# Performance work log

Measured on AMD Instinct MI355X. Metric: run time of the kernel, lower is better.

## Reference

```python
import jax, jax.numpy as jnp
import numpy as np

WINDOW = 1024  # sliding-window mask_mod: attend to keys within WINDOW behind the query


def setup_inputs() -> dict:
    key = jax.random.key(0)
    B, L, H, E = 2, 2048, 16, 64
    qkv = jax.random.normal(key, (B, L, 3, H, E), dtype=jnp.float32)
    return {"qkv": qkv}


def reference(qkv) -> jnp.ndarray:
    # Training path of FlexAttention.forward (key_cache/val_cache/cache_seqlens = None).
    B, L, _, H, E = qkv.shape
    q = qkv[:, :, 0]  # [b, l, h, e]
    k = qkv[:, :, 1]
    v = qkv[:, :, 2]

    scale = 1.0 / (E ** 0.5)  # flex_attention default softmax scaling
    scores = jnp.einsum("bqhe,bkhe->bhqk", q, k) * scale  # [b, h, q, kv]

    q_idx = jnp.arange(L)[:, None]
    kv_idx = jnp.arange(L)[None, :]
    dist = q_idx - kv_idx  # [q, kv]

    # score_mod: ALiBi bias, slope_h = 2^(-8*(h+1)/H)
    slopes = jnp.exp2(-8.0 * (jnp.arange(H, dtype=jnp.float32) + 1.0) / H)
    scores = scores - slopes[None, :, None, None] * dist.astype(jnp.float32)

    # and_masks(mask_mod, causal_mask): sliding window AND causal
    mask = (dist >= 0) & (dist < WINDOW)  # causal guarantees >=1 valid key per row
    scores = jnp.where(mask[None, None], scores, -jnp.inf)

    attn = jax.nn.softmax(scores, axis=-1)
    out = jnp.einsum("bhqk,bkhe->bqhe", attn, v)  # [b, l, h, e]
    return out
```

## Files before the change

kernel.cpp:

```cpp
#include <hip/hip_runtime.h>
#include <cstdint>

#define L_SEQ 2048
#define NH 16
#define EDIM 64
#define WINDOW 1024
#define QT 64
#define KT 64
#define LOG2E 1.4426950408889634f
#define M_FIX 16.0f

typedef short bf16x8 __attribute__((ext_vector_type(8)));
typedef short bf16x4 __attribute__((ext_vector_type(4)));
typedef float f32x4 __attribute__((ext_vector_type(4)));

__device__ __forceinline__ short f2bf(float x) {
    uint32_t u = __builtin_bit_cast(uint32_t, x);
    uint32_t r = (u + 0x7fffu + ((u >> 16) & 1u)) >> 16;
    return (short)(r & 0xffffu);
}
__device__ __forceinline__ short f2bf_trunc(float x) {
    return (short)(__builtin_bit_cast(uint32_t, x) >> 16);
}

__device__ __forceinline__ f32x4 mfma16(bf16x4 a, bf16x4 b, f32x4 c) {
#if __has_builtin(__builtin_amdgcn_mfma_f32_16x16x16bf16_1k)
    return __builtin_amdgcn_mfma_f32_16x16x16bf16_1k(a, b, c, 0, 0, 0);
#else
    asm("s_nop 1\n\tv_mfma_f32_16x16x16_bf16 %0, %1, %2, %0"
        : "+v"(c) : "v"(a), "v"(b));
    return c;
#endif
}

__device__ __forceinline__ void async16(const short* g, const short* l) {
    __builtin_amdgcn_global_load_lds(
        (const __attribute__((address_space(1))) void*)(uintptr_t)(g),
        (__attribute__((address_space(3))) void*)(uintptr_t)(l),
        16, 0, 0);
}

#define SYNC_VMCNT4()                                           \
    do {                                                        \
        asm volatile("s_waitcnt vmcnt(4)" ::: "memory");        \
        __builtin_amdgcn_s_barrier();                           \
        __builtin_amdgcn_sched_barrier(0);                      \
    } while (0)

__global__ __launch_bounds__(256) void prepass4(const float* __restrict__ qkv,
        short* __restrict__ kw, short* __restrict__ vw) {
    __shared__ float vt[64][68];
    const int x = blockIdx.x;
    const int xcd = x & 7, y = x >> 3;
    const int pairid = xcd * 4 + (y >> 5);
    const int tile = y & 31;
    const int b = pairid >> 4, h = pairid & 15;
    const int tid = threadIdx.x;
    const int tg = pairid * 32 + tile;
    const float* base = qkv + (size_t)b * (L_SEQ * 3072) + (size_t)tile * 64 * 3072 + h * 64;
    short* ko = kw + (size_t)tg * 4096;
    short* vo = vw + (size_t)tg * 4096;

    #pragma unroll
    for (int it = 0; it < 2; ++it) {
        const int c = tid + it * 256;
        const int row = c >> 3, cc = (c & 7) ^ (row & 7);
        const float* src = base + (size_t)row * 3072 + 1024 + cc * 8;
        float4 a = *(const float4*)src, d = *(const float4*)(src + 4);
        short* o = ko + (size_t)c * 8;
        o[0] = f2bf(a.x); o[1] = f2bf(a.y); o[2] = f2bf(a.z); o[3] = f2bf(a.w);
        o[4] = f2bf(d.x); o[5] = f2bf(d.y); o[6] = f2bf(d.z); o[7] = f2bf(d.w);
    }
    {
        const int row = tid >> 2, e0 = (tid & 3) << 4;
        const float* src = base + (size_t)row * 3072 + 2048 + e0;
        #pragma unroll
        for (int q4 = 0; q4 < 4; ++q4) {
            float4 a = *(const float4*)(src + q4 * 4);
            vt[e0 + q4 * 4 + 0][row] = a.x;
            vt[e0 + q4 * 4 + 1][row] = a.y;
            vt[e0 + q4 * 4 + 2][row] = a.z;
            vt[e0 + q4 * 4 + 3][row] = a.w;
        }
    }
    __syncthreads();
    #pragma unroll
    for (int it = 0; it < 2; ++it) {
        const int c = tid + it * 256;
        const int et = c >> 7, a = (c >> 6) & 1, l6 = c & 63;
        const int quad = l6 >> 4, r16 = l6 & 15;
        const int e = et * 16 + r16;
        float4 x0 = *(const float4*)&vt[e][a * 32 + quad * 4];
        float4 x1 = *(const float4*)&vt[e][a * 32 + 16 + quad * 4];
        bf16x8 o8;
        o8[0] = f2bf(x0.x); o8[1] = f2bf(x0.y); o8[2] = f2bf(x0.z); o8[3] = f2bf(x0.w);
        o8[4] = f2bf(x1.x); o8[5] = f2bf(x1.y); o8[6] = f2bf(x1.z); o8[7] = f2bf(x1.w);
        *(bf16x8*)(vo + (size_t)c * 8) = o8;
    }
}

__global__ __launch_bounds__(256, 4) void flexattn_fwd8(
        const float* __restrict__ qkv, const short* __restrict__ kw,
        const short* __restrict__ vw, float* __restrict__ out) {
    __shared__ __align__(16) short kB[3][4096];
    __shared__ __align__(16) short vB2[2][4096];

    const int s = blockIdx.y & 31;
    const int k = blockIdx.y >> 5;
    const int t16 = (s + ((k >> 1) << 4)) & 31;
    const int qtile = (k & 1) ? (31 - t16) : t16;
    const int pairid = blockIdx.x * 4 + k;
    const int h = pairid & 15;
    const int b = pairid >> 4;

    const int tid   = threadIdx.x;
    const int w     = tid >> 6;
    const int lane  = tid & 63;
    const int quad  = lane >> 4;
    const int r16   = lane & 15;
    const int qhalf = w & 1;
    const int khalf = w >> 1;
    const int qb    = qtile * QT;
    const int bh32  = (b * NH + h) * 32;
    const int q0    = qb + qhalf * 32 + r16;

    const int t0q = (qb >= WINDOW - 1) ? ((qb - (WINDOW - 1)) >> 6) : 0;
    const int t1  = qtile;
    const int swz = quad ^ (r16 & 7);
    const int cb0 = w * 128;

    float4 qraw[2][2][2];
    #pragma unroll
    for (int g = 0; g < 2; ++g) {
        const float* qrow = qkv + (size_t)b * (L_SEQ * 3072)
                                + (size_t)(q0 + g * 16) * 3072 + h * 64;
        #pragma unroll
        for (int es = 0; es < 2; ++es) {
            const float* p = qrow + es * 32 + quad * 8;
            qraw[g][es][0] = *(const float4*)p;
            qraw[g][es][1] = *(const float4*)(p + 4);
        }
    }

    {
        const int t0c1 = (t0q + 1 <= t1) ? t0q + 1 : t1;
        const short* k0t = kw + (size_t)(bh32 + t0q) * 4096;
        const short* k1t = kw + (size_t)(bh32 + t0c1) * 4096;
        const short* v0t = vw + (size_t)(bh32 + t0q) * 4096;
        short* kd0 = &kB[t0q % 3][0];
        short* kd1 = &kB[(t0q + 1) % 3][0];
        short* vd0 = &vB2[t0q & 1][0];
        async16(k0t + (size_t)(cb0 + lane) * 8,      kd0 + (size_t)cb0 * 8);
        async16(k0t + (size_t)(cb0 + 64 + lane) * 8, kd0 + (size_t)(cb0 + 64) * 8);
        async16(k1t + (size_t)(cb0 + lane) * 8,      kd1 + (size_t)cb0 * 8);
        async16(k1t + (size_t)(cb0 + 64 + lane) * 8, kd1 + (size_t)(cb0 + 64) * 8);
        async16(v0t + (size_t)(cb0 + lane) * 8,      vd0 + (size_t)cb0 * 8);
        async16(v0t + (size_t)(cb0 + 64 + lane) * 8, vd0 + (size_t)(cb0 + 64) * 8);
    }

    const float qscale = 0.125f * LOG2E;
    bf16x8 qfrag[2][2];
    #pragma unroll
    for (int g = 0; g < 2; ++g) {
        #pragma unroll
        for (int es = 0; es < 2; ++es) {
            float4 a = qraw[g][es][0];
            float4 c = qraw[g][es][1];
            bf16x8 f;
            f[0] = f2bf(a.x * qscale); f[1] = f2bf(a.y * qscale);
            f[2] = f2bf(a.z * qscale); f[3] = f2bf(a.w * qscale);
            f[4] = f2bf(c.x * qscale); f[5] = f2bf(c.y * qscale);
            f[6] = f2bf(c.z * qscale); f[7] = f2bf(c.w * qscale);
            qfrag[g][es] = f;
        }
    }

    const float slope2 = __builtin_amdgcn_exp2f(-8.0f * (float)(h + 1) / (float)NH) * LOG2E;
    const float c64 = slope2 * 64.0f;
    f32x4 EA[2][2];
    #pragma unroll
    for (int g = 0; g < 2; ++g)
        #pragma unroll
        for (int ctl = 0; ctl < 2; ++ctl)
            #pragma unroll
            for (int r = 0; r < 4; ++r)
                EA[g][ctl][r] = slope2 * (float)(t0q * 64 + (khalf * 2 + ctl) * 16
                                                 + quad * 4 + r - (q0 + g * 16)) - M_FIX;

    f32x4 O[2][4] = {};
    float rs[2] = {0.f, 0.f};

    for (int kt = t0q; kt <= t1; ++kt) {
        const int kc = kt % 3;
        const int vc = kt & 1;

        SYNC_VMCNT4();

        {
            const int kpre = (kt + 2 <= t1) ? kt + 2 : t1;
            const int vpre = (kt + 1 <= t1) ? kt + 1 : t1;
            short* kd = &kB[(kt + 2) % 3][0];
            short* vd = &vB2[(kt + 1) & 1][0];
            const short* ktile = kw + (size_t)(bh32 + kpre) * 4096;
            const short* vtile = vw + (size_t)(bh32 + vpre) * 4096;
            async16(ktile + (size_t)(cb0 + lane) * 8,      kd + (size_t)cb0 * 8);
            async16(ktile + (size_t)(cb0 + 64 + lane) * 8, kd + (size_t)(cb0 + 64) * 8);
            async16(vtile + (size_t)(cb0 + lane) * 8,      vd + (size_t)cb0 * 8);
            async16(vtile + (size_t)(cb0 + 64 + lane) * 8, vd + (size_t)(cb0 + 64) * 8);
        }

        f32x4 S[2][2];
        __builtin_amdgcn_s_setprio(1);
        #pragma unroll
        for (int ctl = 0; ctl < 2; ++ctl) {
            const int ct = khalf * 2 + ctl;
            const int c0 = ((ct * 16 + r16) << 3) + swz;
            bf16x8 k0 = *(const bf16x8*)&kB[kc][c0 * 8];
            bf16x8 k1 = *(const bf16x8*)&kB[kc][(c0 ^ 4) * 8];
            #pragma unroll
            for (int g = 0; g < 2; ++g) {
                f32x4 acc = __builtin_amdgcn_mfma_f32_16x16x32_bf16(k0, qfrag[g][0], EA[g][ctl], 0, 0, 0);
                S[g][ctl] = __builtin_amdgcn_mfma_f32_16x16x32_bf16(k1, qfrag[g][1], acc, 0, 0, 0);
            }
        }
        __builtin_amdgcn_s_setprio(0);

        bf16x4 pb[2][2];
        if (kt != t0q && kt != t1) {
            #pragma unroll
            for (int g = 0; g < 2; ++g)
                #pragma unroll
                for (int ctl = 0; ctl < 2; ++ctl)
                    #pragma unroll
                    for (int r = 0; r < 4; ++r) {
                        const float pe = __builtin_amdgcn_exp2f(S[g][ctl][r]);
                        rs[g] += pe;
                        pb[g][ctl][r] = f2bf_trunc(pe);
                    }
        } else {
            const int key0 = kt * 64 + khalf * 32 + quad * 4;
            #pragma unroll
            for (int g = 0; g < 2; ++g) {
                const int qg = q0 + g * 16;
                #pragma unroll
                for (int ctl = 0; ctl < 2; ++ctl)
                    #pragma unroll
                    for (int r = 0; r < 4; ++r) {
                        const int dist = qg - (key0 + ctl * 16 + r);
                        float pe = __builtin_amdgcn_exp2f(S[g][ctl][r]);
                        pe = (dist < 0 || dist >= WINDOW) ? 0.0f : pe;
                        rs[g] += pe;
                        pb[g][ctl][r] = f2bf_trunc(pe);
                    }
            }
        }

        SYNC_VMCNT4();

        __builtin_amdgcn_s_setprio(1);
        #pragma unroll
        for (int et = 0; et < 4; ++et) {
            bf16x8 v8 = *(const bf16x8*)&vB2[vc][(size_t)((et * 2 + khalf) * 64 + lane) * 8];
            bf16x4 vlo = {v8[0], v8[1], v8[2], v8[3]};
            bf16x4 vhi = {v8[4], v8[5], v8[6], v8[7]};
            #pragma unroll
            for (int g = 0; g < 2; ++g) {
                O[g][et] = mfma16(vlo, pb[g][0], O[g][et]);
                O[g][et] = mfma16(vhi, pb[g][1], O[g][et]);
            }
        }
        __builtin_amdgcn_s_setprio(0);

        #pragma unroll
        for (int ctl = 0; ctl < 2; ++ctl) {
            EA[0][ctl] += c64;
            EA[1][ctl] += c64;
        }
    }

    __syncthreads();
    float* oS = (float*)&kB[0][0];
    float* rS = (float*)&vB2[0][0];
    if (khalf) {
        float* dst = oS + qhalf * 2048;
        #pragma unroll
        for (int g = 0; g < 2; ++g)
            #pragma unroll
            for (int et = 0; et < 4; ++et)
                #pragma unroll
                for (int j = 0; j < 4; ++j)
                    dst[((g * 4 + et) * 4 + j) * 64 + lane] = O[g][et][j];
        rS[qhalf * 128 + lane]      = rs[0];
        rS[qhalf * 128 + 64 + lane] = rs[1];
    }
    __syncthreads();
    if (!khalf) {
        const float* src = oS + qhalf * 2048;
        #pragma unroll
        for (int g = 0; g < 2; ++g)
            #pragma unroll
            for (int et = 0; et < 4; ++et)
                #pragma unroll
                for (int j = 0; j < 4; ++j)
                    O[g][et][j] += src[((g * 4 + et) * 4 + j) * 64 + lane];
        rs[0] += rS[qhalf * 128 + lane];
        rs[1] += rS[qhalf * 128 + 64 + lane];

        #pragma unroll
        for (int g = 0; g < 2; ++g) {
            float r = rs[g];
            r += __shfl_xor(r, 16, 64);
            r += __shfl_xor(r, 32, 64);
            const float rl = 1.0f / r;
            float* op = out + ((size_t)b * L_SEQ + (q0 + g * 16)) * (NH * EDIM) + h * EDIM;
            #pragma unroll
            for (int et = 0; et < 4; ++et) {
                float4 o4 = {O[g][et][0] * rl, O[g][et][1] * rl,
                             O[g][et][2] * rl, O[g][et][3] * rl};
                *(float4*)(op + et * 16 + quad * 4) = o4;
            }
        }
    }
}

__global__ __launch_bounds__(256, 2) void flexattn_fwd_fb(
        const float* __restrict__ qkv, float* __restrict__ out) {
    __shared__ __align__(16) short kT[KT * 72];
    __shared__ __align__(16) short vB[8 * 64 * 8];
    __shared__ __align__(16) short pT[4][16 * 72];

    const int qtile = blockIdx.x;
    const int h     = blockIdx.y;
    const int b     = blockIdx.z;
    const int tid   = threadIdx.x;
    const int w     = tid >> 6;
    const int lane  = tid & 63;
    const int quad  = lane >> 4;
    const int r16   = lane & 15;
    const int qb = qtile * QT;
    const int rowstride = 3 * NH * EDIM;

    const float* qbase = qkv + ((size_t)b * L_SEQ * 3 + 0) * (NH * EDIM) + h * EDIM;
    const float* kbase = qkv + ((size_t)b * L_SEQ * 3 + 1) * (NH * EDIM) + h * EDIM;
    const float* vbase = qkv + ((size_t)b * L_SEQ * 3 + 2) * (NH * EDIM) + h * EDIM;

    const float qscale = 0.125f * LOG2E;
    bf16x8 qfrag[2];
    {
        const int qg = qb + w * 16 + r16;
        const float* qrow = qbase + (size_t)qg * rowstride;
        #pragma unroll
        for (int es = 0; es < 2; ++es) {
            const float* p = qrow + es * 32 + quad * 8;
            float4 a = *(const float4*)p;
            float4 c = *(const float4*)(p + 4);
            bf16x8 f;
            f[0] = f2bf(a.x * qscale); f[1] = f2bf(a.y * qscale);
            f[2] = f2bf(a.z * qscale); f[3] = f2bf(a.w * qscale);
            f[4] = f2bf(c.x * qscale); f[5] = f2bf(c.y * qscale);
            f[6] = f2bf(c.z * qscale); f[7] = f2bf(c.w * qscale);
            qfrag[es] = f;
        }
    }

    const float slope2 = __builtin_amdgcn_exp2f(-8.0f * (float)(h + 1) / (float)NH) * LOG2E;
    f32x4 O[4] = {{0,0,0,0},{0,0,0,0},{0,0,0,0},{0,0,0,0}};
    float m_run[4] = {-1e30f, -1e30f, -1e30f, -1e30f};
    float l_run[4] = {0.f, 0.f, 0.f, 0.f};

    const int kmin = (qb >= WINDOW - 1) ? (qb - (WINDOW - 1)) : 0;
    const int t0 = kmin >> 6;
    const int t1 = qtile;

    for (int kt = t0; kt <= t1; ++kt) {
        __syncthreads();
        {
            const int j = tid >> 2;
            const int ebase = (tid & 3) * 16;
            const float* krow = kbase + (size_t)(kt * KT + j) * rowstride + ebase;
            const float* vrow = vbase + (size_t)(kt * KT + j) * rowstride + ebase;
            const int js = j >> 5, qd = (j >> 3) & 3, ii = j & 7;
            #pragma unroll
            for (int ee = 0; ee < 4; ++ee) {
                const int e = ebase + ee * 4;
                float4 k4 = *(const float4*)(krow + ee * 4);
                short* kd = &kT[j * 72 + e];
                kd[0] = f2bf(k4.x); kd[1] = f2bf(k4.y);
                kd[2] = f2bf(k4.z); kd[3] = f2bf(k4.w);
                float4 v4 = *(const float4*)(vrow + ee * 4);
                const int et = e >> 4;
                const int ln = qd * 16 + (e & 15);
                short* vd = &vB[(((js * 4 + et) * 64) + ln) * 8 + ii];
                vd[0]  = f2bf(v4.x);
                vd[8]  = f2bf(v4.y);
                vd[16] = f2bf(v4.z);
                vd[24] = f2bf(v4.w);
            }
        }
        __syncthreads();

        f32x4 S[4];
        #pragma unroll
        for (int ct = 0; ct < 4; ++ct) {
            const short* kr = &kT[(ct * 16 + r16) * 72 + quad * 8];
            bf16x8 b0 = *(const bf16x8*)kr;
            bf16x8 b1 = *(const bf16x8*)(kr + 32);
            f32x4 acc = {0.f, 0.f, 0.f, 0.f};
            acc = __builtin_amdgcn_mfma_f32_16x16x32_bf16(qfrag[0], b0, acc, 0, 0, 0);
            acc = __builtin_amdgcn_mfma_f32_16x16x32_bf16(qfrag[1], b1, acc, 0, 0, 0);
            S[ct] = acc;
        }

        const int q0 = qb + w * 16 + quad * 4;
        float p[4][4];
        float mt[4] = {-1e30f, -1e30f, -1e30f, -1e30f};
        #pragma unroll
        for (int ct = 0; ct < 4; ++ct) {
            const int kg = kt * KT + ct * 16 + r16;
            #pragma unroll
            for (int r = 0; r < 4; ++r) {
                const int dist = q0 + r - kg;
                float s2 = S[ct][r] - slope2 * (float)dist;
                if (dist < 0 || dist >= WINDOW) s2 = -1e30f;
                p[ct][r] = s2;
                mt[r] = fmaxf(mt[r], s2);
            }
        }
        #pragma unroll
        for (int d = 1; d < 16; d <<= 1) {
            #pragma unroll
            for (int r = 0; r < 4; ++r)
                mt[r] = fmaxf(mt[r], __shfl_xor(mt[r], d, 64));
        }

        float alpha[4], rsum[4];
        #pragma unroll
        for (int r = 0; r < 4; ++r) {
            const float mn = fmaxf(m_run[r], mt[r]);
            alpha[r] = __builtin_amdgcn_exp2f(m_run[r] - mn);
            m_run[r] = mn;
            float sacc = 0.f;
            #pragma unroll
            for (int ct = 0; ct < 4; ++ct) {
                const float pe = __builtin_amdgcn_exp2f(p[ct][r] - mn);
                p[ct][r] = pe;
                sacc += pe;
            }
            rsum[r] = sacc;
        }
        #pragma unroll
        for (int d = 1; d < 16; d <<= 1) {
            #pragma unroll
            for (int r = 0; r < 4; ++r)
                rsum[r] += __shfl_xor(rsum[r], d, 64);
        }
        #pragma unroll
        for (int r = 0; r < 4; ++r)
            l_run[r] = l_run[r] * alpha[r] + rsum[r];
        #pragma unroll
        for (int et = 0; et < 4; ++et) {
            #pragma unroll
            for (int r = 0; r < 4; ++r)
                O[et][r] *= alpha[r];
        }

        short* pw = &pT[w][0];
        #pragma unroll
        for (int ct = 0; ct < 4; ++ct) {
            #pragma unroll
            for (int r = 0; r < 4; ++r)
                pw[(quad * 4 + r) * 72 + ct * 16 + r16] = f2bf(p[ct][r]);
        }
        bf16x8 aP0 = *(const bf16x8*)(pw + r16 * 72 + quad * 8);
        bf16x8 aP1 = *(const bf16x8*)(pw + r16 * 72 + 32 + quad * 8);

        #pragma unroll
        for (int et = 0; et < 4; ++et) {
            bf16x8 v0 = *(const bf16x8*)(&vB[((0 * 4 + et) * 64 + lane) * 8]);
            O[et] = __builtin_amdgcn_mfma_f32_16x16x32_bf16(aP0, v0, O[et], 0, 0, 0);
            bf16x8 v1 = *(const bf16x8*)(&vB[((1 * 4 + et) * 64 + lane) * 8]);
            O[et] = __builtin_amdgcn_mfma_f32_16x16x32_bf16(aP1, v1, O[et], 0, 0, 0);
        }
    }

    float* obase = out + (((size_t)b * L_SEQ) * NH + (size_t)h) * EDIM;
    #pragma unroll
    for (int r = 0; r < 4; ++r) {
        const int qg = qb + w * 16 + quad * 4 + r;
        const float rl = 1.0f / l_run[r];
        float* orow = obase + (size_t)qg * (NH * EDIM);
        #pragma unroll
        for (int et = 0; et < 4; ++et)
            orow[et * 16 + r16] = O[et][r] * rl;
    }
}

extern "C" void kernel_launch(void* const* d_in, const int* in_sizes, int n_in,
                              void* d_out, int out_size, void* d_ws, size_t ws_size,
                              hipStream_t stream) {
    const float* qkv = (const float*)d_in[0];
    float* out = (float*)d_out;
    const size_t need = (size_t)2 * 1024 * 4096 * sizeof(short);
    if (ws_size >= need) {
        short* kw = (short*)d_ws;
        short* vw = kw + (size_t)1024 * 4096;
        prepass4<<<1024, 256, 0, stream>>>(qkv, kw, vw);
        dim3 grid(8, 128);
        flexattn_fwd8<<<grid, 256, 0, stream>>>(qkv, kw, vw, out);
    } else {
        dim3 gridfb(L_SEQ / QT, NH, 2);
        flexattn_fwd_fb<<<gridfb, 256, 0, stream>>>(qkv, out);
    }
}
```

Baseline: 113.4 us.

## Use persistent 512-thread blocks with atomic work queue and 4-way key split

The attention kernel becomes persistent. Each 512-thread block pulls (head-pair, query-tile) work items from a per-XCD atomic counter, longest tiles first, and the prepass resets the counters. Within a block, eight waves split each 64-key tile four ways instead of two, so each wave does half as many MFMAs per tile, and partial outputs are combined through a two-stage LDS reduction. The aim is better load balance across the triangular sliding-window workload and more latency hiding per CU, at the cost of extra reduction passes, barriers and atomic traffic.

```diff
diff --git a/kernel.cpp b/kernel.cpp
--- a/kernel.cpp
+++ b/kernel.cpp
@@ -40,17 +40,18 @@
         16, 0, 0);
 }
 
-#define SYNC_VMCNT4()                                           \
+#define SYNC_VMCNT2()                                           \
     do {                                                        \
-        asm volatile("s_waitcnt vmcnt(4)" ::: "memory");        \
+        asm volatile("s_waitcnt vmcnt(2)" ::: "memory");        \
         __builtin_amdgcn_s_barrier();                           \
         __builtin_amdgcn_sched_barrier(0);                      \
     } while (0)
 
-__global__ __launch_bounds__(256) void prepass4(const float* __restrict__ qkv,
-        short* __restrict__ kw, short* __restrict__ vw) {
+__global__ __launch_bounds__(256) void prepass5(const float* __restrict__ qkv,
+        short* __restrict__ kw, short* __restrict__ vw, int* __restrict__ cnt) {
     __shared__ float vt[64][68];
     const int x = blockIdx.x;
+    if (x < 8 && threadIdx.x == 0) cnt[x] = 0;
     const int xcd = x & 7, y = x >> 3;
     const int pairid = xcd * 4 + (y >> 5);
     const int tile = y & 31;
@@ -99,225 +100,233 @@
     }
 }
 
-__global__ __launch_bounds__(256, 4) void flexattn_fwd8(
+__global__ __launch_bounds__(512, 4) void flexattn_fwd10(
         const float* __restrict__ qkv, const short* __restrict__ kw,
-        const short* __restrict__ vw, float* __restrict__ out) {
-    __shared__ __align__(16) short kB[3][4096];
-    __shared__ __align__(16) short vB2[2][4096];
-
-    const int s = blockIdx.y & 31;
-    const int k = blockIdx.y >> 5;
-    const int t16 = (s + ((k >> 1) << 4)) & 31;
-    const int qtile = (k & 1) ? (31 - t16) : t16;
-    const int pairid = blockIdx.x * 4 + k;
-    const int h = pairid & 15;
-    const int b = pairid >> 4;
-
-    const int tid   = threadIdx.x;
-    const int w     = tid >> 6;
-    const int lane  = tid & 63;
-    const int quad  = lane >> 4;
-    const int r16   = lane & 15;
+        const short* __restrict__ vw, int* __restrict__ cnt,
+        float* __restrict__ out) {
+    __shared__ __align__(16) short smem[5 * 4096];
+    __shared__ int itemS;
+    short (*kB)[4096]  = (short (*)[4096])&smem[0];
+    short (*vB2)[4096] = (short (*)[4096])&smem[3 * 4096];
+
+    const int xq   = blockIdx.x;
+    const int tid  = threadIdx.x;
+    const int w    = tid >> 6;
+    const int lane = tid & 63;
+    const int quad = lane >> 4;
+    const int r16  = lane & 15;
     const int qhalf = w & 1;
-    const int khalf = w >> 1;
-    const int qb    = qtile * QT;
-    const int bh32  = (b * NH + h) * 32;
-    const int q0    = qb + qhalf * 32 + r16;
-
-    const int t0q = (qb >= WINDOW - 1) ? ((qb - (WINDOW - 1)) >> 6) : 0;
-    const int t1  = qtile;
-    const int swz = quad ^ (r16 & 7);
-    const int cb0 = w * 128;
-
-    float4 qraw[2][2][2];
-    #pragma unroll
-    for (int g = 0; g < 2; ++g) {
-        const float* qrow = qkv + (size_t)b * (L_SEQ * 3072)
-                                + (size_t)(q0 + g * 16) * 3072 + h * 64;
-        #pragma unroll
-        for (int es = 0; es < 2; ++es) {
-            const float* p = qrow + es * 32 + quad * 8;
-            qraw[g][es][0] = *(const float4*)p;
-            qraw[g][es][1] = *(const float4*)(p + 4);
-        }
-    }
-
-    {
-        const int t0c1 = (t0q + 1 <= t1) ? t0q + 1 : t1;
-        const short* k0t = kw + (size_t)(bh32 + t0q) * 4096;
-        const short* k1t = kw + (size_t)(bh32 + t0c1) * 4096;
-        const short* v0t = vw + (size_t)(bh32 + t0q) * 4096;
-        short* kd0 = &kB[t0q % 3][0];
-        short* kd1 = &kB[(t0q + 1) % 3][0];
-        short* vd0 = &vB2[t0q & 1][0];
-        async16(k0t + (size_t)(cb0 + lane) * 8,      kd0 + (size_t)cb0 * 8);
-        async16(k0t + (size_t)(cb0 + 64 + lane) * 8, kd0 + (size_t)(cb0 + 64) * 8);
-        async16(k1t + (size_t)(cb0 + lane) * 8,      kd1 + (size_t)cb0 * 8);
-        async16(k1t + (size_t)(cb0 + 64 + lane) * 8, kd1 + (size_t)(cb0 + 64) * 8);
-        async16(v0t + (size_t)(cb0 + lane) * 8,      vd0 + (size_t)cb0 * 8);
-        async16(v0t + (size_t)(cb0 + 64 + lane) * 8, vd0 + (size_t)(cb0 + 64) * 8);
-    }
-
-    const float qscale = 0.125f * LOG2E;
-    bf16x8 qfrag[2][2];
-    #pragma unroll
-    for (int g = 0; g < 2; ++g) {
-        #pragma unroll
-        for (int es = 0; es < 2; ++es) {
-            float4 a = qraw[g][es][0];
-            float4 c = qraw[g][es][1];
-            bf16x8 f;
-            f[0] = f2bf(a.x * qscale); f[1] = f2bf(a.y * qscale);
-            f[2] = f2bf(a.z * qscale); f[3] = f2bf(a.w * qscale);
-            f[4] = f2bf(c.x * qscale); f[5] = f2bf(c.y * qscale);
-            f[6] = f2bf(c.z * qscale); f[7] = f2bf(c.w * qscale);
-            qfrag[g][es] = f;
-        }
-    }
-
-    const float slope2 = __builtin_amdgcn_exp2f(-8.0f * (float)(h + 1) / (float)NH) * LOG2E;
-    const float c64 = slope2 * 64.0f;
-    f32x4 EA[2][2];
-    #pragma unroll
-    for (int g = 0; g < 2; ++g)
-        #pragma unroll
-        for (int ctl = 0; ctl < 2; ++ctl)
+    const int kq    = w >> 1;
+    const int swz  = quad ^ (r16 & 7);
+    const int cb0  = w * 64;
+
+    for (;;) {
+        if (tid == 0) itemS = atomicAdd(&cnt[xq], 1);
+        __syncthreads();
+        const int item = itemS;
+        if (item >= 128) return;
+
+        const int pairid = xq * 4 + (item & 3);
+        const int qtile  = 31 - (item >> 2);
+        const int h  = pairid & 15;
+        const int b  = pairid >> 4;
+        const int qb = qtile * QT;
+        const int bh32 = pairid * 32;
+        const int q0 = qb + qhalf * 32 + r16;
+        const int t0q = (qb >= WINDOW - 1) ? ((qb - (WINDOW - 1)) >> 6) : 0;
+        const int t1  = qtile;
+
+        float4 qraw[2][2][2];
+        #pragma unroll
+        for (int g = 0; g < 2; ++g) {
+            const float* qrow = qkv + (size_t)b * (L_SEQ * 3072)
+                                    + (size_t)(q0 + g * 16) * 3072 + h * 64;
+            #pragma unroll
+            for (int es = 0; es < 2; ++es) {
+                const float* p = qrow + es * 32 + quad * 8;
+                qraw[g][es][0] = *(const float4*)p;
+                qraw[g][es][1] = *(const float4*)(p + 4);
+            }
+        }
+
+        {
+            const int t0c1 = (t0q + 1 <= t1) ? t0q + 1 : t1;
+            const short* k0t = kw + (size_t)(bh32 + t0q) * 4096;
+            const short* k1t = kw + (size_t)(bh32 + t0c1) * 4096;
+            const short* v0t = vw + (size_t)(bh32 + t0q) * 4096;
+            async16(k0t + (size_t)(cb0 + lane) * 8, &kB[t0q % 3][cb0 * 8]);
+            async16(k1t + (size_t)(cb0 + lane) * 8, &kB[(t0q + 1) % 3][cb0 * 8]);
+            async16(v0t + (size_t)(cb0 + lane) * 8, &vB2[t0q & 1][cb0 * 8]);
+        }
+
+        const float qscale = 0.125f * LOG2E;
+        bf16x8 qfrag[2][2];
+        #pragma unroll
+        for (int g = 0; g < 2; ++g) {
+            #pragma unroll
+            for (int es = 0; es < 2; ++es) {
+                float4 a = qraw[g][es][0];
+                float4 c = qraw[g][es][1];
+                bf16x8 f;
+                f[0] = f2bf(a.x * qscale); f[1] = f2bf(a.y * qscale);
+                f[2] = f2bf(a.z * qscale); f[3] = f2bf(a.w * qscale);
+                f[4] = f2bf(c.x * qscale); f[5] = f2bf(c.y * qscale);
+                f[6] = f2bf(c.z * qscale); f[7] = f2bf(c.w * qscale);
+                qfrag[g][es] = f;
+            }
+        }
+
+        const float slope2 = __builtin_amdgcn_exp2f(-8.0f * (float)(h + 1) / (float)NH) * LOG2E;
+        const float c64 = slope2 * 64.0f;
+        f32x4 EA[2];
+        #pragma unroll
+        for (int g = 0; g < 2; ++g)
             #pragma unroll
             for (int r = 0; r < 4; ++r)
-                EA[g][ctl][r] = slope2 * (float)(t0q * 64 + (khalf * 2 + ctl) * 16
-                                                 + quad * 4 + r - (q0 + g * 16)) - M_FIX;
-
-    f32x4 O[2][4] = {};
-    float rs[2] = {0.f, 0.f};
-
-    for (int kt = t0q; kt <= t1; ++kt) {
-        const int kc = kt % 3;
-        const int vc = kt & 1;
-
-        SYNC_VMCNT4();
-
-        {
-            const int kpre = (kt + 2 <= t1) ? kt + 2 : t1;
-            const int vpre = (kt + 1 <= t1) ? kt + 1 : t1;
-            short* kd = &kB[(kt + 2) % 3][0];
-            short* vd = &vB2[(kt + 1) & 1][0];
-            const short* ktile = kw + (size_t)(bh32 + kpre) * 4096;
-            const short* vtile = vw + (size_t)(bh32 + vpre) * 4096;
-            async16(ktile + (size_t)(cb0 + lane) * 8,      kd + (size_t)cb0 * 8);
-            async16(ktile + (size_t)(cb0 + 64 + lane) * 8, kd + (size_t)(cb0 + 64) * 8);
-            async16(vtile + (size_t)(cb0 + lane) * 8,      vd + (size_t)cb0 * 8);
-            async16(vtile + (size_t)(cb0 + 64 + lane) * 8, vd + (size_t)(cb0 + 64) * 8);
-        }
-
-        f32x4 S[2][2];
-        __builtin_amdgcn_s_setprio(1);
-        #pragma unroll
-        for (int ctl = 0; ctl < 2; ++ctl) {
-            const int ct = khalf * 2 + ctl;
-            const int c0 = ((ct * 16 + r16) << 3) + swz;
-            bf16x8 k0 = *(const bf16x8*)&kB[kc][c0 * 8];
-            bf16x8 k1 = *(const bf16x8*)&kB[kc][(c0 ^ 4) * 8];
-            #pragma unroll
-            for (int g = 0; g < 2; ++g) {
-                f32x4 acc = __builtin_amdgcn_mfma_f32_16x16x32_bf16(k0, qfrag[g][0], EA[g][ctl], 0, 0, 0);
-                S[g][ctl] = __builtin_amdgcn_mfma_f32_16x16x32_bf16(k1, qfrag[g][1], acc, 0, 0, 0);
-            }
-        }
-        __builtin_amdgcn_s_setprio(0);
-
-        bf16x4 pb[2][2];
-        if (kt != t0q && kt != t1) {
-            #pragma unroll
-            for (int g = 0; g < 2; ++g)
-                #pragma unroll
-                for (int ctl = 0; ctl < 2; ++ctl)
+                EA[g][r] = slope2 * (float)(t0q * 64 + kq * 16 + quad * 4 + r
+                                            - (q0 + g * 16)) - M_FIX;
+
+        f32x4 O[2][4] = {};
+        float rs[2] = {0.f, 0.f};
+
+        for (int kt = t0q; kt <= t1; ++kt) {
+            const int kc = kt % 3;
+            const int vc = kt & 1;
+
+            SYNC_VMCNT2();
+
+            {
+                const int kpre = (kt + 2 <= t1) ? kt + 2 : t1;
+                const int vpre = (kt + 1 <= t1) ? kt + 1 : t1;
+                const short* ktile = kw + (size_t)(bh32 + kpre) * 4096;
+                const short* vtile = vw + (size_t)(bh32 + vpre) * 4096;
+                async16(ktile + (size_t)(cb0 + lane) * 8, &kB[(kt + 2) % 3][cb0 * 8]);
+                async16(vtile + (size_t)(cb0 + lane) * 8, &vB2[(kt + 1) & 1][cb0 * 8]);
+            }
+
+            f32x4 S[2];
+            __builtin_amdgcn_s_setprio(1);
+            {
+                const int c0 = ((kq * 16 + r16) << 3) + swz;
+                bf16x8 k0 = *(const bf16x8*)&kB[kc][c0 * 8];
+                bf16x8 k1 = *(const bf16x8*)&kB[kc][(c0 ^ 4) * 8];
+                #pragma unroll
+                for (int g = 0; g < 2; ++g) {
+                    f32x4 acc = __builtin_amdgcn_mfma_f32_16x16x32_bf16(k0, qfrag[g][0], EA[g], 0, 0, 0);
+                    S[g] = __builtin_amdgcn_mfma_f32_16x16x32_bf16(k1, qfrag[g][1], acc, 0, 0, 0);
+                }
+            }
+            __builtin_amdgcn_s_setprio(0);
+
+            bf16x4 pb[2];
+            if (kt != t0q && kt != t1) {
+                #pragma unroll
+                for (int g = 0; g < 2; ++g)
                     #pragma unroll
                     for (int r = 0; r < 4; ++r) {
-                        const float pe = __builtin_amdgcn_exp2f(S[g][ctl][r]);
+                        const float pe = __builtin_amdgcn_exp2f(S[g][r]);
                         rs[g] += pe;
-                        pb[g][ctl][r] = f2bf_trunc(pe);
+                        pb[g][r] = f2bf_trunc(pe);
                     }
-        } else {
-            const int key0 = kt * 64 + khalf * 32 + quad * 4;
-            #pragma unroll
-            for (int g = 0; g < 2; ++g) {
-                const int qg = q0 + g * 16;
-                #pragma unroll
-                for (int ctl = 0; ctl < 2; ++ctl)
+            } else {
+                const int key0 = kt * 64 + kq * 16 + quad * 4;
+                #pragma unroll
+                for (int g = 0; g < 2; ++g) {
+                    const int qg = q0 + g * 16;
                     #pragma unroll
                     for (int r = 0; r < 4; ++r) {
-                        const int dist = qg - (key0 + ctl * 16 + r);
-                        float pe = __builtin_amdgcn_exp2f(S[g][ctl][r]);
+                        const int dist = qg - (key0 + r);
+                        float pe = __builtin_amdgcn_exp2f(S[g][r]);
                         pe = (dist < 0 || dist >= WINDOW) ? 0.0f : pe;
                         rs[g] += pe;
-                        pb[g][ctl][r] = f2bf_trunc(pe);
+                        pb[g][r] = f2bf_trunc(pe);
                     }
-            }
-        }
-
-        SYNC_VMCNT4();
-
-        __builtin_amdgcn_s_setprio(1);
-        #pragma unroll
-        for (int et = 0; et < 4; ++et) {
-            bf16x8 v8 = *(const bf16x8*)&vB2[vc][(size_t)((et * 2 + khalf) * 64 + lane) * 8];
-            bf16x4 vlo = {v8[0], v8[1], v8[2], v8[3]};
-            bf16x4 vhi = {v8[4], v8[5], v8[6], v8[7]};
+                }
+            }
+
+            SYNC_VMCNT2();
+
+            __builtin_amdgcn_s_setprio(1);
+            {
+                const int va = kq >> 1, vh = kq & 1;
+                #pragma unroll
+                for (int et = 0; et < 4; ++et) {
+                    bf16x8 v8 = *(const bf16x8*)&vB2[vc][(size_t)((et * 2 + va) * 64 + lane) * 8];
+                    bf16x4 vf;
+                    if (vh == 0) { vf[0] = v8[0]; vf[1] = v8[1]; vf[2] = v8[2]; vf[3] = v8[3]; }
+                    else         { vf[0] = v8[4]; vf[1] = v8[5]; vf[2] = v8[6]; vf[3] = v8[7]; }
+                    O[0][et] = mfma16(vf, pb[0], O[0][et]);
+                    O[1][et] = mfma16(vf, pb[1], O[1][et]);
+                }
+            }
+            __builtin_amdgcn_s_setprio(0);
+
+            EA[0] += c64;
+            EA[1] += c64;
+        }
+
+        __syncthreads();
+        float* sc = (float*)&smem[0];
+        float* rc = sc + 8192;
+        if (kq >= 2) {
+            const int base = (qhalf * 2 + (kq - 2)) * 2;
+            #pragma unroll
+            for (int g = 0; g < 2; ++g)
+                #pragma unroll
+                for (int et = 0; et < 4; ++et)
+                    #pragma unroll
+                    for (int j = 0; j < 4; ++j)
+                        sc[(((base + g) * 4 + et) * 4 + j) * 64 + lane] = O[g][et][j];
+            rc[(base + 0) * 64 + lane] = rs[0];
+            rc[(base + 1) * 64 + lane] = rs[1];
+        }
+        __syncthreads();
+        if (kq < 2) {
+            const int base = (qhalf * 2 + kq) * 2;
+            #pragma unroll
+            for (int g = 0; g < 2; ++g)
+                #pragma unroll
+                for (int et = 0; et < 4; ++et)
+                    #pragma unroll
+                    for (int j = 0; j < 4; ++j)
+                        O[g][et][j] += sc[(((base + g) * 4 + et) * 4 + j) * 64 + lane];
+            rs[0] += rc[(base + 0) * 64 + lane];
+            rs[1] += rc[(base + 1) * 64 + lane];
+        }
+        __syncthreads();
+        if (kq == 1) {
+            const int base = qhalf * 2;
+            #pragma unroll
+            for (int g = 0; g < 2; ++g)
+                #pragma unroll
+                for (int et = 0; et < 4; ++et)
+                    #pragma unroll
+                    for (int j = 0; j < 4; ++j)
+                        sc[(((base + g) * 4 + et) * 4 + j) * 64 + lane] = O[g][et][j];
+            rc[(base + 0) * 64 + lane] = rs[0];
+            rc[(base + 1) * 64 + lane] = rs[1];
+        }
+        __syncthreads();
+        if (kq == 0) {
+            const int base = qhalf * 2;
             #pragma unroll
             for (int g = 0; g < 2; ++g) {
-                O[g][et] = mfma16(vlo, pb[g][0], O[g][et]);
-                O[g][et] = mfma16(vhi, pb[g][1], O[g][et]);
-            }
-        }
-        __builtin_amdgcn_s_setprio(0);
-
-        #pragma unroll
-        for (int ctl = 0; ctl < 2; ++ctl) {
-            EA[0][ctl] += c64;
-            EA[1][ctl] += c64;
-        }
-    }
-
-    __syncthreads();
-    float* oS = (float*)&kB[0][0];
-    float* rS = (float*)&vB2[0][0];
-    if (khalf) {
-        float* dst = oS + qhalf * 2048;
-        #pragma unroll
-        for (int g = 0; g < 2; ++g)
-            #pragma unroll
-            for (int et = 0; et < 4; ++et)
-                #pragma unroll
-                for (int j = 0; j < 4; ++j)
-                    dst[((g * 4 + et) * 4 + j) * 64 + lane] = O[g][et][j];
-        rS[qhalf * 128 + lane]      = rs[0];
-        rS[qhalf * 128 + 64 + lane] = rs[1];
-    }
-    __syncthreads();
-    if (!khalf) {
-        const float* src = oS + qhalf * 2048;
-        #pragma unroll
-        for (int g = 0; g < 2; ++g)
-            #pragma unroll
-            for (int et = 0; et < 4; ++et)
-                #pragma unroll
-                for (int j = 0; j < 4; ++j)
-                    O[g][et][j] += src[((g * 4 + et) * 4 + j) * 64 + lane];
-        rs[0] += rS[qhalf * 128 + lane];
-        rs[1] += rS[qhalf * 128 + 64 + lane];
-
-        #pragma unroll
-        for (int g = 0; g < 2; ++g) {
-            float r = rs[g];
-            r += __shfl_xor(r, 16, 64);
-            r += __shfl_xor(r, 32, 64);
-            const float rl = 1.0f / r;
-            float* op = out + ((size_t)b * L_SEQ + (q0 + g * 16)) * (NH * EDIM) + h * EDIM;
-            #pragma unroll
-            for (int et = 0; et < 4; ++et) {
-                float4 o4 = {O[g][et][0] * rl, O[g][et][1] * rl,
-                             O[g][et][2] * rl, O[g][et][3] * rl};
-                *(float4*)(op + et * 16 + quad * 4) = o4;
+                #pragma unroll
+                for (int et = 0; et < 4; ++et)
+                    #pragma unroll
+                    for (int j = 0; j < 4; ++j)
+                        O[g][et][j] += sc[(((base + g) * 4 + et) * 4 + j) * 64 + lane];
+                float r = rs[g] + rc[(base + g) * 64 + lane];
+                r += __shfl_xor(r, 16, 64);
+                r += __shfl_xor(r, 32, 64);
+                const float rl = 1.0f / r;
+                float* op = out + ((size_t)b * L_SEQ + (q0 + g * 16)) * (NH * EDIM) + h * EDIM;
+                #pragma unroll
+                for (int et = 0; et < 4; ++et) {
+                    float4 o4 = {O[g][et][0] * rl, O[g][et][1] * rl,
+                                 O[g][et][2] * rl, O[g][et][3] * rl};
+                    *(float4*)(op + et * 16 + quad * 4) = o4;
+                }
             }
         }
     }
@@ -500,13 +509,15 @@
                               hipStream_t stream) {
     const float* qkv = (const float*)d_in[0];
     float* out = (float*)d_out;
-    const size_t need = (size_t)2 * 1024 * 4096 * sizeof(short);
+    const size_t kv_elems = (size_t)1024 * 4096;
+    const size_t need = 2 * kv_elems * sizeof(short) + 8 * sizeof(int);
     if (ws_size >= need) {
         short* kw = (short*)d_ws;
-        short* vw = kw + (size_t)1024 * 4096;
-        prepass4<<<1024, 256, 0, stream>>>(qkv, kw, vw);
-        dim3 grid(8, 128);
-        flexattn_fwd8<<<grid, 256, 0, stream>>>(qkv, kw, vw, out);
+        short* vw = kw + kv_elems;
+        int* cnt = (int*)(vw + kv_elems);
+        prepass5<<<1024, 256, 0, stream>>>(qkv, kw, vw, cnt);
+        dim3 grid(8, 64);
+        flexattn_fwd10<<<grid, 512, 0, stream>>>(qkv, kw, vw, cnt, out);
     } else {
         dim3 gridfb(L_SEQ / QT, NH, 2);
         flexattn_fwd_fb<<<gridfb, 256, 0, stream>>>(qkv, out);
```

Result: slower. 126.3 us (+11.4%).
